# Kernel tuning notes

Measured on AMD Instinct MI355X. Metric: run time of the kernel, lower is better.

Reference implementation:

```python
import jax, jax.numpy as jnp
import numpy as np

NUM_ITERATIONS = 3
EPS = 1e-7


def squash(t, axis=-1):
    # scale = |t|^2/(1+|t|^2), unit = t/sqrt(|t|^2+eps)
    sn = jnp.sum(t * t, axis=axis, keepdims=True)
    return (sn / (1.0 + sn)) * t / jnp.sqrt(sn + EPS)


def setup_inputs() -> dict:
    key = jax.random.key(0)
    kx, kw = jax.random.split(key)
    B, R, CIN = 256, 1152, 8
    C, COUT = 10, 16
    x = jax.random.normal(kx, (B, R, CIN), dtype=jnp.float32)
    W = jax.random.normal(kw, (C, R, CIN, COUT), dtype=jnp.float32)
    return {"x": x, "W": W}


def reference(x, W):
    # u_hat = x[None,:,:,None,:] @ W[:,None]  -> [C, B, R, 1, O]
    u_hat = jnp.einsum('bri,crio->cbro', x, W)[:, :, :, None, :]
    b = jnp.zeros_like(u_hat)  # logits over route nodes, full u_hat shape (faithful)
    outputs = None
    for i in range(NUM_ITERATIONS):
        c = jax.nn.softmax(b, axis=2)  # softmax over route nodes R
        outputs = squash(jnp.sum(c * u_hat, axis=2, keepdims=True))  # [C,B,1,1,O]
        if i != NUM_ITERATIONS - 1:
            # agreement: dot over out channels, broadcast back onto b
            b = b + jnp.sum(u_hat * outputs, axis=-1, keepdims=True)
    return outputs
```

## Files before the change

kernel.cpp:

```cpp
#include <hip/hip_runtime.h>
#include <hip/hip_fp16.h>

#define RDIM 1152
#define CIN  8
#define COUT 16
#define CDIM 10
#define BDIM 256
#define EPS 1e-7f

#define ARB 64
#define ABB 32
#define NRBLK (RDIM / ARB)
#define NBBLK (BDIM / ABB)
#define ANWG (CDIM * NRBLK * NBBLK)
#define WSTRIDE 136

__global__ __launch_bounds__(256) void caps_uhat(
    const float* __restrict__ x, const float* __restrict__ W,
    __half* __restrict__ uh)
{
    const int orig = blockIdx.x;
    const int id   = (orig & 7) * (ANWG / 8) + (orig >> 3);
    const int c    = id % CDIM;
    const int chnk = id / CDIM;
    const int rblk = chnk >> 3;
    const int bblk = chnk & 7;
    const int r0   = rblk * ARB;
    const int b0   = bblk * ABB;

    const int t  = threadIdx.x;
    const int oq = t & 3;
    const int rl = t >> 2;

    __shared__ float wlds[ARB * WSTRIDE];

    {
        const float* wsrc = W + ((size_t)c * RDIM + r0) * (CIN * COUT);
        #pragma unroll
        for (int k = 0; k < 8; ++k) {
            const int idx = t + k * 256;
            const int row = idx >> 5;
            const int col = idx & 31;
            float4 w4 = *(const float4*)(wsrc + row * (CIN * COUT) + col * 4);
            *(float4*)&wlds[row * WSTRIDE + col * 4] = w4;
        }
    }
    __syncthreads();

    float wreg[CIN][4];
    #pragma unroll
    for (int i = 0; i < CIN; ++i) {
        float4 w4 = *(const float4*)&wlds[rl * WSTRIDE + i * COUT + oq * 4];
        wreg[i][0] = w4.x; wreg[i][1] = w4.y; wreg[i][2] = w4.z; wreg[i][3] = w4.w;
    }

    const float* xbase = x + ((size_t)b0 * RDIM + r0 + rl) * CIN;
    __half* ubase = uh + (((size_t)c * BDIM + b0) * RDIM + r0 + rl) * COUT + oq * 4;

    #pragma unroll 4
    for (int bl = 0; bl < ABB; ++bl) {
        const float4* xp = (const float4*)(xbase + (size_t)bl * RDIM * CIN);
        float4 p0 = xp[0], p1 = xp[1];
        float xr[CIN] = {p0.x, p0.y, p0.z, p0.w, p1.x, p1.y, p1.z, p1.w};

        float a0 = 0.f, a1 = 0.f, a2 = 0.f, a3 = 0.f;
        #pragma unroll
        for (int i = 0; i < CIN; ++i) {
            a0 = fmaf(xr[i], wreg[i][0], a0);
            a1 = fmaf(xr[i], wreg[i][1], a1);
            a2 = fmaf(xr[i], wreg[i][2], a2);
            a3 = fmaf(xr[i], wreg[i][3], a3);
        }
        __half2 h0 = __floats2half2_rn(a0, a1), h1 = __floats2half2_rn(a2, a3);
        *(uint2*)(ubase + (size_t)bl * RDIM * COUT) =
            make_uint2(*(const unsigned*)&h0, *(const unsigned*)&h1);
    }
}

#define BUNIT 18

__global__ __launch_bounds__(256) void caps_route2(
    const __half* __restrict__ uh, float* __restrict__ out)
{
    const int cb   = blockIdx.x;
    const int t    = threadIdx.x;
    const int lane = t & 63;
    const int wave = t >> 6;
    const int oq   = t & 3;
    const int rsub = t >> 2;

    __shared__ uint2 uhs[RDIM * COUT / 4];
    __shared__ float red[4][20];
    __shared__ __align__(16) float vout[COUT];

    const uint4* src = (const uint4*)(uh + (size_t)cb * RDIM * COUT);
    uint4* dst = (uint4*)uhs;
    float sp[8] = {0.f, 0.f, 0.f, 0.f, 0.f, 0.f, 0.f, 0.f};
    #pragma unroll
    for (int k = 0; k < 9; ++k) {
        uint4 v = src[t + k * 256];
        dst[t + k * 256] = v;
        float2 f0 = __half22float2(*(const __half2*)&v.x);
        float2 f1 = __half22float2(*(const __half2*)&v.y);
        float2 f2 = __half22float2(*(const __half2*)&v.z);
        float2 f3 = __half22float2(*(const __half2*)&v.w);
        sp[0] += f0.x; sp[1] += f0.y; sp[2] += f1.x; sp[3] += f1.y;
        sp[4] += f2.x; sp[5] += f2.y; sp[6] += f3.x; sp[7] += f3.y;
    }
    #pragma unroll
    for (int off = 2; off <= 32; off <<= 1) {
        #pragma unroll
        for (int j = 0; j < 8; ++j) sp[j] += __shfl_xor(sp[j], off);
    }
    if (lane < 2) {
        #pragma unroll
        for (int j = 0; j < 8; ++j) red[wave][lane * 8 + j] = sp[j];
    }
    __syncthreads();

    if (wave == 0 && lane < COUT) {
        float s = 0.f;
        #pragma unroll
        for (int w2 = 0; w2 < 4; ++w2) s += red[w2][lane];
        s *= (1.0f / (float)RDIM);
        float sn = s * s;
        #pragma unroll
        for (int off = 1; off < 16; off <<= 1) sn += __shfl_xor(sn, off);
        const float scale = (sn / (1.0f + sn)) / sqrtf(sn + EPS);
        vout[lane] = s * scale;
    }
    __syncthreads();

    float bb[BUNIT];
    #pragma unroll
    for (int k = 0; k < BUNIT; ++k) bb[k] = 0.f;

    #pragma unroll
    for (int it = 1; it <= 2; ++it) {
        const float4 vq = *(const float4*)&vout[oq * 4];
        float Zp = 0.f, s0 = 0.f, s1 = 0.f, s2 = 0.f, s3 = 0.f;
        #pragma unroll
        for (int k = 0; k < BUNIT; ++k) {
            const int r = k * 64 + rsub;
            uint2 raw = uhs[r * 4 + oq];
            float2 fA = __half22float2(*(const __half2*)&raw.x);
            float2 fB = __half22float2(*(const __half2*)&raw.y);
            float a = fA.x * vq.x;
            a = fmaf(fA.y, vq.y, a);
            a = fmaf(fB.x, vq.z, a);
            a = fmaf(fB.y, vq.w, a);
            a += __shfl_xor(a, 1);
            a += __shfl_xor(a, 2);
            bb[k] += a;
            float e = __expf(bb[k]);
            Zp += e;
            s0 = fmaf(e, fA.x, s0); s1 = fmaf(e, fA.y, s1);
            s2 = fmaf(e, fB.x, s2); s3 = fmaf(e, fB.y, s3);
        }
        #pragma unroll
        for (int off = 32; off >= 4; off >>= 1) {
            Zp += __shfl_xor(Zp, off);
            s0 += __shfl_xor(s0, off);
            s1 += __shfl_xor(s1, off);
            s2 += __shfl_xor(s2, off);
            s3 += __shfl_xor(s3, off);
        }
        if (lane < 4) {
            red[wave][lane * 4 + 0] = s0;
            red[wave][lane * 4 + 1] = s1;
            red[wave][lane * 4 + 2] = s2;
            red[wave][lane * 4 + 3] = s3;
            if (lane == 0) red[wave][16] = Zp;
        }
        __syncthreads();
        if (wave == 0 && lane < COUT) {
            float Z = 0.f;
            #pragma unroll
            for (int w2 = 0; w2 < 4; ++w2) Z += red[w2][16];
            float s = 0.f;
            #pragma unroll
            for (int w2 = 0; w2 < 4; ++w2) s += red[w2][lane];
            s /= Z;
            float sn = s * s;
            #pragma unroll
            for (int off = 1; off < 16; off <<= 1) sn += __shfl_xor(sn, off);
            const float scale = (sn / (1.0f + sn)) / sqrtf(sn + EPS);
            vout[lane] = s * scale;
        }
        __syncthreads();
    }

    if (t < 4) {
        float* op = out + (size_t)cb * COUT + t * 4;
        *(float4*)op = *(const float4*)&vout[t * 4];
    }
}

#define NB   2
#define FBLOCK 384
#define FUNITS 12
#define FNW (FBLOCK / 64)
#define NPAIR (BDIM / NB)
#define FNWG (CDIM * NPAIR)

__global__ __launch_bounds__(FBLOCK) void caps_route_fused(
    const float* __restrict__ x, const float* __restrict__ W,
    float* __restrict__ out)
{
    const int orig = blockIdx.x;
    const int wg   = (orig & 7) * (FNWG / 8) + (orig >> 3);
    const int c    = wg / NPAIR;
    const int b0   = (wg % NPAIR) * NB;
    const int tid  = threadIdx.x;
    const int lane = tid & 63;
    const int wave = tid >> 6;
    const int oq   = tid & 3;
    const int rsub = tid >> 2;

    __shared__ uint2 uhT[NB][4][1156];
    __shared__ float red[NB][FNW][COUT];
    __shared__ float scalz[NB][FNW];
    __shared__ __align__(16) float vout[NB][COUT];

    const float* __restrict__ Wc  = W + (size_t)c * RDIM * CIN * COUT;
    const float* __restrict__ xb0 = x + (size_t)b0 * RDIM * CIN;
    const float* __restrict__ xb1 = xb0 + RDIM * CIN;

    #pragma unroll
    for (int k = 0; k < FUNITS; ++k) {
        const int r = k * 96 + rsub;
        const float4* xq0 = (const float4*)(xb0 + (size_t)r * CIN);
        const float4* xq1 = (const float4*)(xb1 + (size_t)r * CIN);
        float4 p00 = xq0[0], p01 = xq0[1];
        float4 p10 = xq1[0], p11 = xq1[1];
        float xr0[CIN] = {p00.x, p00.y, p00.z, p00.w, p01.x, p01.y, p01.z, p01.w};
        float xr1[CIN] = {p10.x, p10.y, p10.z, p10.w, p11.x, p11.y, p11.z, p11.w};
        const float* wrow = Wc + (size_t)r * (CIN * COUT) + oq * 4;
        float a00 = 0.f, a01 = 0.f, a02 = 0.f, a03 = 0.f;
        float a10 = 0.f, a11 = 0.f, a12 = 0.f, a13 = 0.f;
        #pragma unroll
        for (int i = 0; i < CIN; ++i) {
            float4 w = *(const float4*)(wrow + i * COUT);
            a00 = fmaf(xr0[i], w.x, a00); a01 = fmaf(xr0[i], w.y, a01);
            a02 = fmaf(xr0[i], w.z, a02); a03 = fmaf(xr0[i], w.w, a03);
            a10 = fmaf(xr1[i], w.x, a10); a11 = fmaf(xr1[i], w.y, a11);
            a12 = fmaf(xr1[i], w.z, a12); a13 = fmaf(xr1[i], w.w, a13);
        }
        __half2 hA0 = __floats2half2_rn(a00, a01), hB0 = __floats2half2_rn(a02, a03);
        __half2 hA1 = __floats2half2_rn(a10, a11), hB1 = __floats2half2_rn(a12, a13);
        uhT[0][oq][r] = make_uint2(*(const unsigned*)&hA0, *(const unsigned*)&hB0);
        uhT[1][oq][r] = make_uint2(*(const unsigned*)&hA1, *(const unsigned*)&hB1);
    }
    __syncthreads();

    float bb0[FUNITS], bb1[FUNITS];
    #pragma unroll
    for (int k = 0; k < FUNITS; ++k) { bb0[k] = 0.f; bb1[k] = 0.f; }

    #pragma unroll
    for (int it = 0; it < 3; ++it) {
        float Zp0 = 0.f, s00 = 0.f, s01 = 0.f, s02 = 0.f, s03 = 0.f;
        float Zp1 = 0.f, s10 = 0.f, s11 = 0.f, s12 = 0.f, s13 = 0.f;
        #pragma unroll
        for (int k = 0; k < FUNITS; ++k) {
            const int r = k * 96 + rsub;
            float e0 = __expf(bb0[k]);
            float e1 = __expf(bb1[k]);
            uint2 r0 = uhT[0][oq][r], r1 = uhT[1][oq][r];
            float2 fA0 = __half22float2(*(const __half2*)&r0.x);
            float2 fB0 = __half22float2(*(const __half2*)&r0.y);
            float2 fA1 = __half22float2(*(const __half2*)&r1.x);
            float2 fB1 = __half22float2(*(const __half2*)&r1.y);
            Zp0 += e0; Zp1 += e1;
            s00 = fmaf(e0, fA0.x, s00); s01 = fmaf(e0, fA0.y, s01);
            s02 = fmaf(e0, fB0.x, s02); s03 = fmaf(e0, fB0.y, s03);
            s10 = fmaf(e1, fA1.x, s10); s11 = fmaf(e1, fA1.y, s11);
            s12 = fmaf(e1, fB1.x, s12); s13 = fmaf(e1, fB1.y, s13);
        }
        #pragma unroll
        for (int off = 32; off >= 4; off >>= 1) {
            Zp0 += __shfl_xor(Zp0, off);  Zp1 += __shfl_xor(Zp1, off);
            s00 += __shfl_xor(s00, off);  s10 += __shfl_xor(s10, off);
            s01 += __shfl_xor(s01, off);  s11 += __shfl_xor(s11, off);
            s02 += __shfl_xor(s02, off);  s12 += __shfl_xor(s12, off);
            s03 += __shfl_xor(s03, off);  s13 += __shfl_xor(s13, off);
        }
        if (lane < 4) {
            red[0][wave][lane * 4 + 0] = s00; red[0][wave][lane * 4 + 1] = s01;
            red[0][wave][lane * 4 + 2] = s02; red[0][wave][lane * 4 + 3] = s03;
            red[1][wave][lane * 4 + 0] = s10; red[1][wave][lane * 4 + 1] = s11;
            red[1][wave][lane * 4 + 2] = s12; red[1][wave][lane * 4 + 3] = s13;
            if (lane == 0) { scalz[0][wave] = Zp0; scalz[1][wave] = Zp1; }
        }
        __syncthreads();
        if (wave == 0 && (lane & 31) < COUT) {
            const int nb = lane >> 5;
            const int o  = lane & 15;
            float Z = 0.f;
            #pragma unroll
            for (int w2 = 0; w2 < FNW; ++w2) Z += scalz[nb][w2];
            float s = 0.f;
            #pragma unroll
            for (int w2 = 0; w2 < FNW; ++w2) s += red[nb][w2][o];
            s /= Z;
            float sn = s * s;
            #pragma unroll
            for (int off = 1; off < 16; off <<= 1) sn += __shfl_xor(sn, off);
            const float scale = (sn / (1.0f + sn)) / sqrtf(sn + EPS);
            vout[nb][o] = s * scale;
        }
        __syncthreads();
        if (it < 2) {
            const float4 v0 = *(const float4*)&vout[0][oq * 4];
            const float4 v1 = *(const float4*)&vout[1][oq * 4];
            #pragma unroll
            for (int k = 0; k < FUNITS; ++k) {
                const int r = k * 96 + rsub;
                uint2 r0 = uhT[0][oq][r], r1 = uhT[1][oq][r];
                float2 fA0 = __half22float2(*(const __half2*)&r0.x);
                float2 fB0 = __half22float2(*(const __half2*)&r0.y);
                float2 fA1 = __half22float2(*(const __half2*)&r1.x);
                float2 fB1 = __half22float2(*(const __half2*)&r1.y);
                float a0 = fA0.x * v0.x;
                a0 = fmaf(fA0.y, v0.y, a0);
                a0 = fmaf(fB0.x, v0.z, a0);
                a0 = fmaf(fB0.y, v0.w, a0);
                float a1 = fA1.x * v1.x;
                a1 = fmaf(fA1.y, v1.y, a1);
                a1 = fmaf(fB1.x, v1.z, a1);
                a1 = fmaf(fB1.y, v1.w, a1);
                a0 += __shfl_xor(a0, 1);  a1 += __shfl_xor(a1, 1);
                a0 += __shfl_xor(a0, 2);  a1 += __shfl_xor(a1, 2);
                bb0[k] += a0;
                bb1[k] += a1;
            }
        }
    }
    if (tid < 8) {
        const int nb = tid >> 2, q = tid & 3;
        float* op = out + ((size_t)c * BDIM + b0 + nb) * COUT + q * 4;
        *(float4*)op = *(const float4*)&vout[nb][q * 4];
    }
}

extern "C" void kernel_launch(void* const* d_in, const int* in_sizes, int n_in,
                              void* d_out, int out_size, void* d_ws, size_t ws_size,
                              hipStream_t stream) {
    const float* x = (const float*)d_in[0];
    const float* W = (const float*)d_in[1];
    float* out = (float*)d_out;

    const size_t UH_BYTES = (size_t)CDIM * BDIM * RDIM * COUT * sizeof(__half);
    if (ws_size >= UH_BYTES) {
        __half* uh = (__half*)d_ws;
        caps_uhat<<<ANWG, 256, 0, stream>>>(x, W, uh);
        caps_route2<<<CDIM * BDIM, 256, 0, stream>>>(uh, out);
    } else {
        caps_route_fused<<<FNWG, FBLOCK, 0, stream>>>(x, W, out);
    }
}
```

Baseline: 56.28 us.

## Stage x in LDS and keep W in registers for u_hat kernel

Reworks the u_hat kernel so that each thread loads its W slice (8 inputs by 8 outputs) straight from global memory into registers, while the x tile is staged in LDS and shared across threads. Each thread now computes 8 outputs per batch row and writes 16-byte half-precision stores. The batch tile is halved and the grid doubled. The aim is to cut redundant global x loads and to use wider stores. In exchange, W is read more often (each block loads it for only 16 batches) and register pressure rises; empty asm statements pin the W registers.

```diff
diff --git a/kernel.cpp b/kernel.cpp
--- a/kernel.cpp
+++ b/kernel.cpp
@@ -9,11 +9,11 @@
 #define EPS 1e-7f
 
 #define ARB 64
-#define ABB 32
+#define ABB 16
 #define NRBLK (RDIM / ARB)
 #define NBBLK (BDIM / ABB)
 #define ANWG (CDIM * NRBLK * NBBLK)
-#define WSTRIDE 136
+#define XSTRIDE 12
 
 __global__ __launch_bounds__(256) void caps_uhat(
     const float* __restrict__ x, const float* __restrict__ W,
@@ -23,57 +23,101 @@
     const int id   = (orig & 7) * (ANWG / 8) + (orig >> 3);
     const int c    = id % CDIM;
     const int chnk = id / CDIM;
-    const int rblk = chnk >> 3;
-    const int bblk = chnk & 7;
+    const int rblk = chnk >> 4;
+    const int bblk = chnk & 15;
     const int r0   = rblk * ARB;
     const int b0   = bblk * ABB;
 
-    const int t  = threadIdx.x;
-    const int oq = t & 3;
-    const int rl = t >> 2;
-
-    __shared__ float wlds[ARB * WSTRIDE];
+    const int t    = threadIdx.x;
+    const int half = t >> 7;
+    const int u    = t & 127;
+    const int rl   = u >> 1;
+    const int oh   = u & 1;
+
+    __shared__ float xs[ABB * ARB * XSTRIDE];
 
     {
-        const float* wsrc = W + ((size_t)c * RDIM + r0) * (CIN * COUT);
+        const float* xsrc = x + ((size_t)b0 * RDIM + r0) * CIN;
         #pragma unroll
         for (int k = 0; k < 8; ++k) {
-            const int idx = t + k * 256;
-            const int row = idx >> 5;
-            const int col = idx & 31;
-            float4 w4 = *(const float4*)(wsrc + row * (CIN * COUT) + col * 4);
-            *(float4*)&wlds[row * WSTRIDE + col * 4] = w4;
-        }
-    }
+            const int uu = t + k * 256;
+            const int bl = uu >> 7;
+            const int q  = uu & 127;
+            float4 v = *(const float4*)(xsrc + (size_t)bl * RDIM * CIN + q * 4);
+            *(float4*)&xs[(bl * ARB + (q >> 1)) * XSTRIDE + (q & 1) * 4] = v;
+        }
+    }
+
+    float w0[8], w1[8], w2[8], w3[8], w4[8], w5[8], w6[8], w7[8];
+    {
+        const float* wb = W + ((size_t)c * RDIM + r0 + rl) * (CIN * COUT) + oh * 8;
+        #define LDW(I, DST)                                                   \
+        {                                                                     \
+            float4 lo = *(const float4*)(wb + (I) * COUT);                    \
+            float4 hi = *(const float4*)(wb + (I) * COUT + 4);                \
+            DST[0] = lo.x; DST[1] = lo.y; DST[2] = lo.z; DST[3] = lo.w;       \
+            DST[4] = hi.x; DST[5] = hi.y; DST[6] = hi.z; DST[7] = hi.w;       \
+        }
+        LDW(0, w0) LDW(1, w1) LDW(2, w2) LDW(3, w3)
+        LDW(4, w4) LDW(5, w5) LDW(6, w6) LDW(7, w7)
+        #undef LDW
+    }
+    asm volatile("" :
+        "+v"(w0[0]), "+v"(w0[1]), "+v"(w0[2]), "+v"(w0[3]),
+        "+v"(w0[4]), "+v"(w0[5]), "+v"(w0[6]), "+v"(w0[7]),
+        "+v"(w1[0]), "+v"(w1[1]), "+v"(w1[2]), "+v"(w1[3]),
+        "+v"(w1[4]), "+v"(w1[5]), "+v"(w1[6]), "+v"(w1[7]));
+    asm volatile("" :
+        "+v"(w2[0]), "+v"(w2[1]), "+v"(w2[2]), "+v"(w2[3]),
+        "+v"(w2[4]), "+v"(w2[5]), "+v"(w2[6]), "+v"(w2[7]),
+        "+v"(w3[0]), "+v"(w3[1]), "+v"(w3[2]), "+v"(w3[3]),
+        "+v"(w3[4]), "+v"(w3[5]), "+v"(w3[6]), "+v"(w3[7]));
+    asm volatile("" :
+        "+v"(w4[0]), "+v"(w4[1]), "+v"(w4[2]), "+v"(w4[3]),
+        "+v"(w4[4]), "+v"(w4[5]), "+v"(w4[6]), "+v"(w4[7]),
+        "+v"(w5[0]), "+v"(w5[1]), "+v"(w5[2]), "+v"(w5[3]),
+        "+v"(w5[4]), "+v"(w5[5]), "+v"(w5[6]), "+v"(w5[7]));
+    asm volatile("" :
+        "+v"(w6[0]), "+v"(w6[1]), "+v"(w6[2]), "+v"(w6[3]),
+        "+v"(w6[4]), "+v"(w6[5]), "+v"(w6[6]), "+v"(w6[7]),
+        "+v"(w7[0]), "+v"(w7[1]), "+v"(w7[2]), "+v"(w7[3]),
+        "+v"(w7[4]), "+v"(w7[5]), "+v"(w7[6]), "+v"(w7[7]));
+
     __syncthreads();
 
-    float wreg[CIN][4];
-    #pragma unroll
-    for (int i = 0; i < CIN; ++i) {
-        float4 w4 = *(const float4*)&wlds[rl * WSTRIDE + i * COUT + oq * 4];
-        wreg[i][0] = w4.x; wreg[i][1] = w4.y; wreg[i][2] = w4.z; wreg[i][3] = w4.w;
-    }
-
-    const float* xbase = x + ((size_t)b0 * RDIM + r0 + rl) * CIN;
-    __half* ubase = uh + (((size_t)c * BDIM + b0) * RDIM + r0 + rl) * COUT + oq * 4;
-
-    #pragma unroll 4
-    for (int bl = 0; bl < ABB; ++bl) {
-        const float4* xp = (const float4*)(xbase + (size_t)bl * RDIM * CIN);
-        float4 p0 = xp[0], p1 = xp[1];
-        float xr[CIN] = {p0.x, p0.y, p0.z, p0.w, p1.x, p1.y, p1.z, p1.w};
-
-        float a0 = 0.f, a1 = 0.f, a2 = 0.f, a3 = 0.f;
-        #pragma unroll
-        for (int i = 0; i < CIN; ++i) {
-            a0 = fmaf(xr[i], wreg[i][0], a0);
-            a1 = fmaf(xr[i], wreg[i][1], a1);
-            a2 = fmaf(xr[i], wreg[i][2], a2);
-            a3 = fmaf(xr[i], wreg[i][3], a3);
-        }
+    __half* ubase = uh + (((size_t)c * BDIM + b0 + half * 8) * RDIM + r0 + rl) * COUT
+                  + oh * 8;
+    const size_t ustep = (size_t)RDIM * COUT;
+    const float* xrow = &xs[(half * 8 * ARB + rl) * XSTRIDE];
+
+    #pragma unroll
+    for (int bl = 0; bl < ABB / 2; ++bl) {
+        const float* xp = xrow + bl * (ARB * XSTRIDE);
+        float4 p0 = *(const float4*)(xp);
+        float4 p1 = *(const float4*)(xp + 4);
+
+        float a0 = p0.x * w0[0];
+        float a1 = p0.x * w0[1];
+        float a2 = p0.x * w0[2];
+        float a3 = p0.x * w0[3];
+        float a4 = p0.x * w0[4];
+        float a5 = p0.x * w0[5];
+        float a6 = p0.x * w0[6];
+        float a7 = p0.x * w0[7];
+        #define FMA8(XI, WR)                                                  \
+            a0 = fmaf((XI), WR[0], a0); a1 = fmaf((XI), WR[1], a1);           \
+            a2 = fmaf((XI), WR[2], a2); a3 = fmaf((XI), WR[3], a3);           \
+            a4 = fmaf((XI), WR[4], a4); a5 = fmaf((XI), WR[5], a5);           \
+            a6 = fmaf((XI), WR[6], a6); a7 = fmaf((XI), WR[7], a7);
+        FMA8(p0.y, w1) FMA8(p0.z, w2) FMA8(p0.w, w3)
+        FMA8(p1.x, w4) FMA8(p1.y, w5) FMA8(p1.z, w6) FMA8(p1.w, w7)
+        #undef FMA8
+
         __half2 h0 = __floats2half2_rn(a0, a1), h1 = __floats2half2_rn(a2, a3);
-        *(uint2*)(ubase + (size_t)bl * RDIM * COUT) =
-            make_uint2(*(const unsigned*)&h0, *(const unsigned*)&h1);
+        __half2 h2 = __floats2half2_rn(a4, a5), h3 = __floats2half2_rn(a6, a7);
+        uint4 packed = make_uint4(*(const unsigned*)&h0, *(const unsigned*)&h1,
+                                  *(const unsigned*)&h2, *(const unsigned*)&h3);
+        *(uint4*)(ubase + bl * ustep) = packed;
     }
 }
 
```

Result: no change. 56.14 us (-0.3%).
